# Kernel optimization log

Measured on AMD Instinct MI355X. Metric: run time of the kernel, lower is better.

The kernel has to match this reference:

```python
import jax, jax.numpy as jnp
import numpy as np

B_SZ, C_DIM, N_DIM, S_DIM, L = 4, 512, 512, 64, 8192


def setup_inputs() -> dict:
    key = jax.random.key(0)
    ks = jax.random.split(key, 6)
    inp = jax.random.normal(ks[0], (B_SZ, C_DIM, L), dtype=jnp.float32)
    # dtA_real must be negative (exponential decay) so exp(dtA_real * l) stays bounded for l up to L
    dtA_real = -jax.random.uniform(ks[1], (N_DIM, S_DIM), dtype=jnp.float32, minval=1e-4, maxval=1e-2)
    dtA_imag = jax.random.uniform(ks[2], (N_DIM, S_DIM), dtype=jnp.float32, minval=0.0, maxval=0.1)
    Bm = jax.random.normal(ks[3], (N_DIM, C_DIM), dtype=jnp.float32) / np.float32(np.sqrt(C_DIM))
    Cm = jax.random.normal(ks[4], (C_DIM, N_DIM), dtype=jnp.float32) / np.float32(np.sqrt(N_DIM))
    E = jax.random.normal(ks[5], (N_DIM, S_DIM), dtype=jnp.float32) / np.float32(np.sqrt(S_DIM))
    return {"input": inp, "dtA_real": dtA_real, "dtA_imag": dtA_imag, "B": Bm, "C": Cm, "E": E}


def _synth_kernel(dtA_real, dtA_imag, E, length):
    # _K with complex_proj=False, weight=E, dim=-2:
    # K[n, s, l] = exp(dtA_real[n,s] * l) * cos(dtA_imag[n,s] * l); reduce over s with weight E.
    lrange = jnp.arange(length, dtype=jnp.float32)
    K = jnp.exp(dtA_real[..., None] * lrange) * jnp.cos(dtA_imag[..., None] * lrange)  # [n, s, L]
    return jnp.sum(K * E[..., None], axis=-2)  # [n, L]


def _fft_conv_dw(u, k, n):
    # real FFT causal (zero-padded to 2n) depthwise convolution: y = irfft(rfft(u) * rfft(k))[:n]
    uf = jnp.fft.rfft(u, 2 * n)          # [b, n, n+1] complex
    kf = jnp.fft.rfft(k, 2 * n)          # [n, n+1] complex, broadcast over batch
    return jnp.fft.irfft(uf * kf, 2 * n)[..., :n]


def reference(input, dtA_real, dtA_imag, B, C, E):
    n = input.shape[-1]
    # kernel synthesis (cached + detached in the torch module)
    K = jax.lax.stop_gradient(_synth_kernel(dtA_real, dtA_imag, E, n))  # [n_dim, L]
    x = jnp.einsum('bcl,nc->bnl', input, B)   # input projection
    x = _fft_conv_dw(x, K, n)                  # depthwise long conv
    return jnp.einsum('bnl,dn->bdl', x, C)     # output projection
```

## Files before the change

### kernel.cpp

```cpp
#include <hip/hip_runtime.h>
#include <hip/hip_bf16.h>

typedef unsigned short u16;
typedef __attribute__((ext_vector_type(8))) short short8;
typedef __attribute__((ext_vector_type(8))) unsigned short ushort8v;
typedef __attribute__((ext_vector_type(4))) float floatx4;

#define BSZ   4
#define CDIM  512
#define NDIM  512
#define SDIM  64
#define LEN   8192

__device__ __forceinline__ u16 f2bf(float x) {
    unsigned int u = __float_as_uint(x);
    unsigned int r = (u + 0x7FFFu + ((u >> 16) & 1u)) >> 16;
    return (u16)r;
}

#define GLL16(g, l)                                                          \
    __builtin_amdgcn_global_load_lds(                                        \
        (const __attribute__((address_space(1))) unsigned int*)(g),          \
        (__attribute__((address_space(3))) unsigned int*)(l), 16, 0, 0)

__global__ __launch_bounds__(256) void prep_nw(const float* __restrict__ dAr,
                                               const float* __restrict__ dAi,
                                               const float* __restrict__ E,
                                               u16* __restrict__ Af,
                                               u16* __restrict__ WW,
                                               const float* __restrict__ Bmf,
                                               const float* __restrict__ Cmf,
                                               u16* __restrict__ bh,
                                               u16* __restrict__ ch) {
    __shared__ float sA[64], sW[64], sE[64];
    __shared__ float Ms[128][65];
    __shared__ float sK[128];
    const int n = blockIdx.x;
    const int t = threadIdx.x;
    if (t < 64) {
        sA[t] = dAr[n * 64 + t];
        sW[t] = dAi[n * 64 + t];
        sE[t] = E[n * 64 + t];
    }
    {
        int i = n * 512 + t * 2;
        float2 vb = *(const float2*)&Bmf[i];
        float2 vc = *(const float2*)&Cmf[i];
        ushort2 hb, hc;
        hb.x = f2bf(vb.x); hb.y = f2bf(vb.y);
        hc.x = f2bf(vc.x); hc.y = f2bf(vc.y);
        *(ushort2*)&bh[i] = hb;
        *(ushort2*)&ch[i] = hc;
    }
    __syncthreads();
    u16* Afn = Af + (size_t)n * 32768;
#pragma unroll 4
    for (int it = 0; it < 32; ++it) {
        int idx = it * 256 + t;
        int tt = idx >> 6, s = idx & 63;
        float a = sA[s], w = sW[s], e = sE[s];
        float tp1 = (float)(tt + 1);
        float sn, cs;
        __sincosf(w * tp1, &sn, &cs);
        float ea = __expf(a * tp1) * e;
        float mr = ea * cs;
        Ms[tt][s] = mr;
        Afn[tt * 256 + 128 + s] = f2bf(mr);
        Afn[tt * 256 + 192 + s] = f2bf(-ea * sn);
    }
    __syncthreads();
    if (t < 128) {
        float acc = 0.f;
        if (t == 0) {
#pragma unroll
            for (int s = 0; s < 64; ++s) acc += sE[s];
        } else {
#pragma unroll
            for (int s = 0; s < 64; ++s) acc += Ms[t - 1][s];
        }
        sK[t] = acc;
    }
    __syncthreads();
#pragma unroll 8
    for (int it = 0; it < 64; ++it) {
        int idx = it * 256 + t;
        int tt = idx >> 7, k = idx & 127;
        float v = (k <= tt) ? sK[tt - k] : 0.f;
        Afn[tt * 256 + k] = f2bf(v);
    }
    u16* WWn = WW + (size_t)n * 16384;
#pragma unroll 4
    for (int it = 0; it < 32; ++it) {
        int idx = it * 256 + t;
        int s = idx >> 7, tau = idx & 127;
        float a = sA[s], w = sW[s];
        float d = (float)(127 - tau);
        float sn, cs;
        __sincosf(w * d, &sn, &cs);
        float ea = __expf(a * d);
        WWn[s * 128 + tau] = f2bf(ea * cs);
        WWn[(s + 64) * 128 + tau] = f2bf(ea * sn);
    }
}

__global__ __launch_bounds__(256) void transpose_in(const float* __restrict__ src,
                                                    u16* __restrict__ dst) {
    __shared__ float tile[64][65];
    const int b  = blockIdx.z;
    const int r0 = blockIdx.y * 64;
    const int c0 = blockIdx.x * 64;
    const int t  = threadIdx.x;
    const float* s = src + (size_t)b * 512 * 8192;
#pragma unroll
    for (int p = 0; p < 4; ++p) {
        int r = (t >> 4) + p * 16;
        float4 v = *(const float4*)&s[(size_t)(r0 + r) * 8192 + c0 + (t & 15) * 4];
        tile[r][(t & 15) * 4 + 0] = v.x;
        tile[r][(t & 15) * 4 + 1] = v.y;
        tile[r][(t & 15) * 4 + 2] = v.z;
        tile[r][(t & 15) * 4 + 3] = v.w;
    }
    __syncthreads();
#pragma unroll
    for (int p = 0; p < 4; ++p) {
        int i  = (t >> 4) + p * 16;
        int cb = (t & 15) * 4;
        ushort4 h;
        u16* hp = (u16*)&h;
#pragma unroll
        for (int q = 0; q < 4; ++q) hp[q] = f2bf(tile[cb + q][i]);
        *(ushort4*)&dst[((size_t)b * 8192 + c0 + i) * 512 + r0 + cb] = h;
    }
}

__global__ __launch_bounds__(256) void transpose_u16(const u16* __restrict__ src,
                                                     u16* __restrict__ dst) {
    __shared__ u16 tile[64][72];
    const int b  = blockIdx.z;
    const int n0 = blockIdx.y * 64;
    const int l0 = blockIdx.x * 64;
    const int t  = threadIdx.x;
    const u16* s = src + (size_t)b * 512 * 8192;
    u16* d = dst + (size_t)b * 8192 * 512;
#pragma unroll
    for (int p = 0; p < 2; ++p) {
        int r = (t >> 3) + p * 32;
        *(ushort8v*)&tile[r][(t & 7) * 8] =
            *(const ushort8v*)&s[(size_t)(n0 + r) * 8192 + l0 + (t & 7) * 8];
    }
    __syncthreads();
#pragma unroll
    for (int p = 0; p < 2; ++p) {
        int li = (t >> 3) + p * 32;
        int cb = (t & 7) * 8;
        ushort8v v;
#pragma unroll
        for (int q = 0; q < 8; ++q) v[q] = tile[cb + q][li];
        *(ushort8v*)&d[(size_t)(l0 + li) * 512 + n0 + cb] = v;
    }
}

__global__ __launch_bounds__(256) void gemm_bf16_o16(const u16* __restrict__ A,
                                                     const u16* __restrict__ Xt,
                                                     u16* __restrict__ Y) {
    __shared__ u16 As[128 * 32];
    __shared__ u16 Xs[128 * 32];
    const int b    = blockIdx.z;
    const int m0   = blockIdx.y * 128;
    const int l0   = blockIdx.x * 128;
    const int t    = threadIdx.x;
    const int w    = t >> 6;
    const int lane = t & 63;
    const int mq   = (w >> 1) * 64;
    const int lq   = (w & 1) * 64;
    const u16* Xb = Xt + (size_t)b * 8192 * 512;
    const size_t a_off = (size_t)(m0 + 32 * w + (lane >> 2)) * 512 + (lane & 3) * 8;
    const size_t x_off = (size_t)(l0 + 32 * w + (lane >> 2)) * 512 + (lane & 3) * 8;
    u16* AsW = As + w * 1024;
    u16* XsW = Xs + w * 1024;

    floatx4 acc[4][4];
#pragma unroll
    for (int i = 0; i < 4; ++i)
#pragma unroll
        for (int j = 0; j < 4; ++j) acc[i][j] = (floatx4)0.f;
    const int fr = lane & 15;
    const int fk = (lane >> 4) * 8;

    for (int k0 = 0; k0 < 512; k0 += 32) {
        __syncthreads();
        GLL16(A + a_off + k0, AsW);
        GLL16(A + a_off + 16 * 512 + k0, AsW + 512);
        GLL16(Xb + x_off + k0, XsW);
        GLL16(Xb + x_off + 16 * 512 + k0, XsW + 512);
        __syncthreads();
        short8 af[4], bf[4];
#pragma unroll
        for (int i = 0; i < 4; ++i) {
            af[i] = *(const short8*)&As[(mq + i * 16 + fr) * 32 + fk];
            bf[i] = *(const short8*)&Xs[(lq + i * 16 + fr) * 32 + fk];
        }
#pragma unroll
        for (int i = 0; i < 4; ++i)
#pragma unroll
            for (int j = 0; j < 4; ++j)
                acc[i][j] = __builtin_amdgcn_mfma_f32_16x16x32_bf16(
                    af[i], bf[j], acc[i][j], 0, 0, 0);
    }
    u16* Yb = Y + (size_t)b * 512 * 8192;
#pragma unroll
    for (int i = 0; i < 4; ++i)
#pragma unroll
        for (int j = 0; j < 4; ++j)
#pragma unroll
            for (int r = 0; r < 4; ++r) {
                int mg = m0 + mq + i * 16 + (lane >> 4) * 4 + r;
                int lg = l0 + lq + j * 16 + (lane & 15);
                Yb[(size_t)mg * 8192 + lg] = f2bf(acc[i][j][r]);
            }
}

__global__ __launch_bounds__(256) void gemm_bf16_o32(const u16* __restrict__ A,
                                                     const u16* __restrict__ Xt,
                                                     float* __restrict__ Y) {
    __shared__ u16 As[128 * 32];
    __shared__ u16 Xs[128 * 32];
    const int b    = blockIdx.z;
    const int m0   = blockIdx.y * 128;
    const int l0   = blockIdx.x * 128;
    const int t    = threadIdx.x;
    const int w    = t >> 6;
    const int lane = t & 63;
    const int mq   = (w >> 1) * 64;
    const int lq   = (w & 1) * 64;
    const u16* Xb = Xt + (size_t)b * 8192 * 512;
    const size_t a_off = (size_t)(m0 + 32 * w + (lane >> 2)) * 512 + (lane & 3) * 8;
    const size_t x_off = (size_t)(l0 + 32 * w + (lane >> 2)) * 512 + (lane & 3) * 8;
    u16* AsW = As + w * 1024;
    u16* XsW = Xs + w * 1024;

    floatx4 acc[4][4];
#pragma unroll
    for (int i = 0; i < 4; ++i)
#pragma unroll
        for (int j = 0; j < 4; ++j) acc[i][j] = (floatx4)0.f;
    const int fr = lane & 15;
    const int fk = (lane >> 4) * 8;

    for (int k0 = 0; k0 < 512; k0 += 32) {
        __syncthreads();
        GLL16(A + a_off + k0, AsW);
        GLL16(A + a_off + 16 * 512 + k0, AsW + 512);
        GLL16(Xb + x_off + k0, XsW);
        GLL16(Xb + x_off + 16 * 512 + k0, XsW + 512);
        __syncthreads();
        short8 af[4], bf[4];
#pragma unroll
        for (int i = 0; i < 4; ++i) {
            af[i] = *(const short8*)&As[(mq + i * 16 + fr) * 32 + fk];
            bf[i] = *(const short8*)&Xs[(lq + i * 16 + fr) * 32 + fk];
        }
#pragma unroll
        for (int i = 0; i < 4; ++i)
#pragma unroll
            for (int j = 0; j < 4; ++j)
                acc[i][j] = __builtin_amdgcn_mfma_f32_16x16x32_bf16(
                    af[i], bf[j], acc[i][j], 0, 0, 0);
    }
    float* Yb = Y + (size_t)b * 512 * 8192;
#pragma unroll
    for (int i = 0; i < 4; ++i)
#pragma unroll
        for (int j = 0; j < 4; ++j)
#pragma unroll
            for (int r = 0; r < 4; ++r) {
                int mg = m0 + mq + i * 16 + (lane >> 4) * 4 + r;
                int lg = l0 + lq + j * 16 + (lane & 15);
                Yb[(size_t)mg * 8192 + lg] = acc[i][j][r];
            }
}

__global__ __launch_bounds__(256) void se_gemm(const u16* __restrict__ xbf,
                                               const u16* __restrict__ WW,
                                               u16* __restrict__ SEf) {
    __shared__ u16 As[128 * 32];
    __shared__ u16 Bs[128 * 32];
    const int n  = blockIdx.y;
    const int c0 = blockIdx.x * 128;
    const int t  = threadIdx.x;
    const int w  = t >> 6, lane = t & 63;
    const int mq = (w >> 1) * 64;
    const int lq = (w & 1) * 64;
    const int ar0 = 32 * w + (lane >> 2);
    const int kq8 = (lane & 3) * 8;
    const int c_a0 = c0 + ar0, c_a1 = c_a0 + 16;
    const size_t xrow0 = ((size_t)(c_a0 >> 6) * 512 + n) * 8192 + (size_t)(c_a0 & 63) * 128 + kq8;
    const size_t xrow1 = ((size_t)(c_a1 >> 6) * 512 + n) * 8192 + (size_t)(c_a1 & 63) * 128 + kq8;
    const size_t brow0 = (size_t)n * 16384 + (size_t)ar0 * 128 + kq8;
    const size_t brow1 = brow0 + 16 * 128;
    const int wofs = w * 1024;

    floatx4 acc[4][4];
#pragma unroll
    for (int i = 0; i < 4; ++i)
#pragma unroll
        for (int j = 0; j < 4; ++j) acc[i][j] = (floatx4)0.f;
    const int fr = lane & 15, fk = (lane >> 4) * 8;

    for (int k0 = 0; k0 < 128; k0 += 32) {
        __syncthreads();
        GLL16(xbf + xrow0 + k0, As + wofs);
        GLL16(xbf + xrow1 + k0, As + wofs + 512);
        GLL16(WW + brow0 + k0, Bs + wofs);
        GLL16(WW + brow1 + k0, Bs + wofs + 512);
        __syncthreads();
        short8 af[4], bf[4];
#pragma unroll
        for (int i = 0; i < 4; ++i) {
            af[i] = *(const short8*)&As[(mq + i * 16 + fr) * 32 + fk];
            bf[i] = *(const short8*)&Bs[(lq + i * 16 + fr) * 32 + fk];
        }
#pragma unroll
        for (int i = 0; i < 4; ++i)
#pragma unroll
            for (int j = 0; j < 4; ++j)
                acc[i][j] = __builtin_amdgcn_mfma_f32_16x16x32_bf16(
                    af[i], bf[j], acc[i][j], 0, 0, 0);
    }
#pragma unroll
    for (int i = 0; i < 4; ++i)
#pragma unroll
        for (int j = 0; j < 4; ++j)
#pragma unroll
            for (int r = 0; r < 4; ++r) {
                int c = c0 + mq + i * 16 + (lane >> 4) * 4 + r;
                int q = lq + j * 16 + (lane & 15);
                SEf[(((size_t)(c >> 6) * 512 + n) * 64 + (c & 63)) * 128 + q] =
                    f2bf(acc[i][j][r]);
            }
}

__global__ __launch_bounds__(256) void bscan(const float* __restrict__ dAr,
                                             const float* __restrict__ dAi,
                                             const u16* __restrict__ SEf,
                                             u16* __restrict__ Ht) {
    const int id = blockIdx.x * 256 + threadIdx.x;
    const int s = id & 63, n = (id >> 6) & 511, b = id >> 15;
    const float a = dAr[n * 64 + s], wv = dAi[n * 64 + s];
    const float eaT = expf(a * 128.f);
    float sT, cT;
    sincosf(wv * 128.f, &sT, &cT);
    const float zTr = eaT * cT, zTi = eaT * sT;
    const size_t base = ((size_t)b * 512 + n) * 64 * 128;
    float Hr = 0.f, Hi = 0.f;
    for (int j = 0; j < 64; ++j) {
        Ht[base + j * 128 + s]      = f2bf(Hr);
        Ht[base + j * 128 + 64 + s] = f2bf(Hi);
        float ser = __uint_as_float((unsigned int)SEf[base + j * 128 + s] << 16);
        float sei = __uint_as_float((unsigned int)SEf[base + j * 128 + 64 + s] << 16);
        float nHr = fmaf(zTr, Hr, fmaf(-zTi, Hi, ser));
        float nHi = fmaf(zTi, Hr, fmaf(zTr, Hi, sei));
        Hr = nHr; Hi = nHi;
    }
}

__global__ __launch_bounds__(256) void y_gemm(const u16* __restrict__ xbf,
                                              const u16* __restrict__ Ht,
                                              const u16* __restrict__ Af,
                                              u16* __restrict__ wyb) {
    __shared__ u16 As[128 * 32];
    __shared__ u16 Bs[128 * 32];
    const int n  = blockIdx.y;
    const int c0 = blockIdx.x * 128;
    const int t  = threadIdx.x;
    const int w  = t >> 6, lane = t & 63;
    const int mq = (w >> 1) * 64;
    const int lq = (w & 1) * 64;
    const int ar0 = 32 * w + (lane >> 2);
    const int kq8 = (lane & 3) * 8;
    const int c_a0 = c0 + ar0, c_a1 = c_a0 + 16;
    const size_t xrow0 = ((size_t)(c_a0 >> 6) * 512 + n) * 8192 + (size_t)(c_a0 & 63) * 128 + kq8;
    const size_t xrow1 = ((size_t)(c_a1 >> 6) * 512 + n) * 8192 + (size_t)(c_a1 & 63) * 128 + kq8;
    const size_t hrow0 = (((size_t)(c_a0 >> 6) * 512 + n) * 64 + (c_a0 & 63)) * 128 + kq8;
    const size_t hrow1 = (((size_t)(c_a1 >> 6) * 512 + n) * 64 + (c_a1 & 63)) * 128 + kq8;
    const size_t brow0 = (size_t)n * 32768 + (size_t)ar0 * 256 + kq8;
    const size_t brow1 = brow0 + 16 * 256;
    const int wofs = w * 1024;

    floatx4 acc[4][4];
#pragma unroll
    for (int i = 0; i < 4; ++i)
#pragma unroll
        for (int j = 0; j < 4; ++j) acc[i][j] = (floatx4)0.f;
    const int fr = lane & 15, fk = (lane >> 4) * 8;

    for (int k0 = 0; k0 < 256; k0 += 32) {
        __syncthreads();
        if (k0 < 128) {
            GLL16(xbf + xrow0 + k0, As + wofs);
            GLL16(xbf + xrow1 + k0, As + wofs + 512);
        } else {
            GLL16(Ht + hrow0 + (k0 - 128), As + wofs);
            GLL16(Ht + hrow1 + (k0 - 128), As + wofs + 512);
        }
        GLL16(Af + brow0 + k0, Bs + wofs);
        GLL16(Af + brow1 + k0, Bs + wofs + 512);
        __syncthreads();
        short8 af[4], bf[4];
#pragma unroll
        for (int i = 0; i < 4; ++i) {
            af[i] = *(const short8*)&As[(mq + i * 16 + fr) * 32 + fk];
            bf[i] = *(const short8*)&Bs[(lq + i * 16 + fr) * 32 + fk];
        }
#pragma unroll
        for (int i = 0; i < 4; ++i)
#pragma unroll
            for (int j = 0; j < 4; ++j)
                acc[i][j] = __builtin_amdgcn_mfma_f32_16x16x32_bf16(
                    af[i], bf[j], acc[i][j], 0, 0, 0);
    }
#pragma unroll
    for (int i = 0; i < 4; ++i)
#pragma unroll
        for (int j = 0; j < 4; ++j)
#pragma unroll
            for (int r = 0; r < 4; ++r) {
                int c  = c0 + mq + i * 16 + (lane >> 4) * 4 + r;
                int tc = lq + j * 16 + (lane & 15);
                wyb[((size_t)(c >> 6) * 512 + n) * 8192 + (size_t)(c & 63) * 128 + tc] =
                    f2bf(acc[i][j][r]);
            }
}

extern "C" void kernel_launch(void* const* d_in, const int* in_sizes, int n_in,
                              void* d_out, int out_size, void* d_ws, size_t ws_size,
                              hipStream_t stream) {
    const float* input = (const float*)d_in[0];
    const float* dAr   = (const float*)d_in[1];
    const float* dAi   = (const float*)d_in[2];
    const float* Bm    = (const float*)d_in[3];
    const float* Cm    = (const float*)d_in[4];
    const float* E     = (const float*)d_in[5];
    float* out = (float*)d_out;

    char* ws = (char*)d_ws;
    const size_t MB = 1048576;
    u16* xt   = (u16*)(ws + 0);
    u16* xbf  = (u16*)(ws + 32 * MB);
    u16* Af   = (u16*)(ws + 64 * MB);
    u16* WW   = (u16*)(ws + 96 * MB);
    u16* SEf  = (u16*)(ws + 112 * MB);
    u16* Ht   = (u16*)(ws + 144 * MB);
    u16* Bmb  = (u16*)(ws + 176 * MB);
    u16* Cmb  = (u16*)(ws + 177 * MB);
    u16* wyb  = xt;
    u16* yt   = xbf;

    prep_nw<<<512, 256, 0, stream>>>(dAr, dAi, E, Af, WW, Bm, Cm, Bmb, Cmb);
    transpose_in<<<dim3(128, 8, BSZ), 256, 0, stream>>>(input, xt);
    gemm_bf16_o16<<<dim3(64, 4, BSZ), 256, 0, stream>>>(Bmb, xt, xbf);
    se_gemm<<<dim3(2, 512), 256, 0, stream>>>(xbf, WW, SEf);
    bscan<<<512, 256, 0, stream>>>(dAr, dAi, SEf, Ht);
    y_gemm<<<dim3(2, 512), 256, 0, stream>>>(xbf, Ht, Af, wyb);
    transpose_u16<<<dim3(128, 8, BSZ), 256, 0, stream>>>(wyb, yt);
    gemm_bf16_o32<<<dim3(64, 4, BSZ), 256, 0, stream>>>(Cmb, yt, out);
}
```

Baseline: 271.0 us.

## Double GEMM K-tile to 64 with XOR-swizzled LDS layout

Both projection GEMMs now stage 64-wide K slices per iteration instead of 32, halving the number of barrier pairs per tile. Global columns are XOR-swizzled by row when loaded directly into LDS, and fragment reads apply the matching swizzle, so MFMA operand reads avoid LDS bank conflicts on the wider rows. LDS use per block doubles, which could reduce occupancy.

Result: no change. 268.1 us (-1.1%).

```diff
diff --git a/kernel.cpp b/kernel.cpp
--- a/kernel.cpp
+++ b/kernel.cpp
@@ -163,8 +163,8 @@
 __global__ __launch_bounds__(256) void gemm_bf16_o16(const u16* __restrict__ A,
                                                      const u16* __restrict__ Xt,
                                                      u16* __restrict__ Y) {
-    __shared__ u16 As[128 * 32];
-    __shared__ u16 Xs[128 * 32];
+    __shared__ u16 As[128 * 64];
+    __shared__ u16 Xs[128 * 64];
     const int b    = blockIdx.z;
     const int m0   = blockIdx.y * 128;
     const int l0   = blockIdx.x * 128;
@@ -174,10 +174,11 @@
     const int mq   = (w >> 1) * 64;
     const int lq   = (w & 1) * 64;
     const u16* Xb = Xt + (size_t)b * 8192 * 512;
-    const size_t a_off = (size_t)(m0 + 32 * w + (lane >> 2)) * 512 + (lane & 3) * 8;
-    const size_t x_off = (size_t)(l0 + 32 * w + (lane >> 2)) * 512 + (lane & 3) * 8;
-    u16* AsW = As + w * 1024;
-    u16* XsW = Xs + w * 1024;
+    const int scol = (((lane & 7) ^ (lane >> 3)) << 3);
+    const size_t a_off = (size_t)(m0 + 32 * w + (lane >> 3)) * 512 + scol;
+    const size_t x_off = (size_t)(l0 + 32 * w + (lane >> 3)) * 512 + scol;
+    u16* AsW = As + w * 2048;
+    u16* XsW = Xs + w * 2048;
 
     floatx4 acc[4][4];
 #pragma unroll
@@ -186,26 +187,32 @@
         for (int j = 0; j < 4; ++j) acc[i][j] = (floatx4)0.f;
     const int fr = lane & 15;
     const int fk = (lane >> 4) * 8;
-
-    for (int k0 = 0; k0 < 512; k0 += 32) {
-        __syncthreads();
-        GLL16(A + a_off + k0, AsW);
-        GLL16(A + a_off + 16 * 512 + k0, AsW + 512);
-        GLL16(Xb + x_off + k0, XsW);
-        GLL16(Xb + x_off + 16 * 512 + k0, XsW + 512);
-        __syncthreads();
-        short8 af[4], bf[4];
-#pragma unroll
-        for (int i = 0; i < 4; ++i) {
-            af[i] = *(const short8*)&As[(mq + i * 16 + fr) * 32 + fk];
-            bf[i] = *(const short8*)&Xs[(lq + i * 16 + fr) * 32 + fk];
-        }
-#pragma unroll
-        for (int i = 0; i < 4; ++i)
-#pragma unroll
-            for (int j = 0; j < 4; ++j)
-                acc[i][j] = __builtin_amdgcn_mfma_f32_16x16x32_bf16(
-                    af[i], bf[j], acc[i][j], 0, 0, 0);
+    const int swz = (fr & 7) << 3;
+
+    for (int k0 = 0; k0 < 512; k0 += 64) {
+        __syncthreads();
+#pragma unroll
+        for (int g = 0; g < 4; ++g) {
+            GLL16(A + a_off + g * 4096 + k0, AsW + g * 512);
+            GLL16(Xb + x_off + g * 4096 + k0, XsW + g * 512);
+        }
+        __syncthreads();
+#pragma unroll
+        for (int kk = 0; kk < 64; kk += 32) {
+            short8 af[4], bf[4];
+            const int pc = (kk + fk) ^ swz;
+#pragma unroll
+            for (int i = 0; i < 4; ++i) {
+                af[i] = *(const short8*)&As[(mq + i * 16 + fr) * 64 + pc];
+                bf[i] = *(const short8*)&Xs[(lq + i * 16 + fr) * 64 + pc];
+            }
+#pragma unroll
+            for (int i = 0; i < 4; ++i)
+#pragma unroll
+                for (int j = 0; j < 4; ++j)
+                    acc[i][j] = __builtin_amdgcn_mfma_f32_16x16x32_bf16(
+                        af[i], bf[j], acc[i][j], 0, 0, 0);
+        }
     }
     u16* Yb = Y + (size_t)b * 512 * 8192;
 #pragma unroll
@@ -223,8 +230,8 @@
 __global__ __launch_bounds__(256) void gemm_bf16_o32(const u16* __restrict__ A,
                                                      const u16* __restrict__ Xt,
                                                      float* __restrict__ Y) {
-    __shared__ u16 As[128 * 32];
-    __shared__ u16 Xs[128 * 32];
+    __shared__ u16 As[128 * 64];
+    __shared__ u16 Xs[128 * 64];
     const int b    = blockIdx.z;
     const int m0   = blockIdx.y * 128;
     const int l0   = blockIdx.x * 128;
@@ -234,10 +241,11 @@
     const int mq   = (w >> 1) * 64;
     const int lq   = (w & 1) * 64;
     const u16* Xb = Xt + (size_t)b * 8192 * 512;
-    const size_t a_off = (size_t)(m0 + 32 * w + (lane >> 2)) * 512 + (lane & 3) * 8;
-    const size_t x_off = (size_t)(l0 + 32 * w + (lane >> 2)) * 512 + (lane & 3) * 8;
-    u16* AsW = As + w * 1024;
-    u16* XsW = Xs + w * 1024;
+    const int scol = (((lane & 7) ^ (lane >> 3)) << 3);
+    const size_t a_off = (size_t)(m0 + 32 * w + (lane >> 3)) * 512 + scol;
+    const size_t x_off = (size_t)(l0 + 32 * w + (lane >> 3)) * 512 + scol;
+    u16* AsW = As + w * 2048;
+    u16* XsW = Xs + w * 2048;
 
     floatx4 acc[4][4];
 #pragma unroll
@@ -246,26 +254,32 @@
         for (int j = 0; j < 4; ++j) acc[i][j] = (floatx4)0.f;
     const int fr = lane & 15;
     const int fk = (lane >> 4) * 8;
-
-    for (int k0 = 0; k0 < 512; k0 += 32) {
-        __syncthreads();
-        GLL16(A + a_off + k0, AsW);
-        GLL16(A + a_off + 16 * 512 + k0, AsW + 512);
-        GLL16(Xb + x_off + k0, XsW);
-        GLL16(Xb + x_off + 16 * 512 + k0, XsW + 512);
-        __syncthreads();
-        short8 af[4], bf[4];
-#pragma unroll
-        for (int i = 0; i < 4; ++i) {
-            af[i] = *(const short8*)&As[(mq + i * 16 + fr) * 32 + fk];
-            bf[i] = *(const short8*)&Xs[(lq + i * 16 + fr) * 32 + fk];
-        }
-#pragma unroll
-        for (int i = 0; i < 4; ++i)
-#pragma unroll
-            for (int j = 0; j < 4; ++j)
-                acc[i][j] = __builtin_amdgcn_mfma_f32_16x16x32_bf16(
-                    af[i], bf[j], acc[i][j], 0, 0, 0);
+    const int swz = (fr & 7) << 3;
+
+    for (int k0 = 0; k0 < 512; k0 += 64) {
+        __syncthreads();
+#pragma unroll
+        for (int g = 0; g < 4; ++g) {
+            GLL16(A + a_off + g * 4096 + k0, AsW + g * 512);
+            GLL16(Xb + x_off + g * 4096 + k0, XsW + g * 512);
+        }
+        __syncthreads();
+#pragma unroll
+        for (int kk = 0; kk < 64; kk += 32) {
+            short8 af[4], bf[4];
+            const int pc = (kk + fk) ^ swz;
+#pragma unroll
+            for (int i = 0; i < 4; ++i) {
+                af[i] = *(const short8*)&As[(mq + i * 16 + fr) * 64 + pc];
+                bf[i] = *(const short8*)&Xs[(lq + i * 16 + fr) * 64 + pc];
+            }
+#pragma unroll
+            for (int i = 0; i < 4; ++i)
+#pragma unroll
+                for (int j = 0; j < 4; ++j)
+                    acc[i][j] = __builtin_amdgcn_mfma_f32_16x16x32_bf16(
+                        af[i], bf[j], acc[i][j], 0, 0, 0);
+        }
     }
     float* Yb = Y + (size_t)b * 512 * 8192;
 #pragma unroll
```
